# Kernel tuning notes

Hardware: AMD Instinct MI355X
Metric: run time of the kernel (lower is better)

Reference implementation:

```python
import jax, jax.numpy as jnp
import numpy as np

N_NODES = 4096
IN_FEAT = 256
N_HEADS = 8
N_HIDDEN = 32  # out_features // n_heads
NEG_SLOPE = 0.2


def setup_inputs() -> dict:
    key = jax.random.key(0)
    k1, k2, k3, k4 = jax.random.split(key, 4)
    h = jax.random.normal(k1, (N_NODES, IN_FEAT), dtype=jnp.float32)
    W = jax.random.normal(k2, (N_HEADS * N_HIDDEN, IN_FEAT), dtype=jnp.float32) * 0.05
    a = jax.random.normal(k3, (2 * N_HIDDEN,), dtype=jnp.float32) * 0.05
    adj_mat = jax.random.randint(k4, (N_NODES, N_NODES, 1), 0, 2, dtype=jnp.int32)
    return {"h": h, "W": W, "a": a, "adj_mat": adj_mat}


def reference(h, W, a, adj_mat):
    n = h.shape[0]
    # g = linear(h) -> [N, H, F]
    g = (h @ W.T).reshape(n, N_HEADS, N_HIDDEN)
    # e_ij = LeakyReLU(a^T [g_i || g_j]) = LeakyReLU(a_l . g_i + a_r . g_j)
    a_l, a_r = a[:N_HIDDEN], a[N_HIDDEN:]
    s_i = jnp.einsum('nhf,f->nh', g, a_l)  # destination term (repeat_interleave axis)
    s_j = jnp.einsum('nhf,f->nh', g, a_r)  # source term (repeat axis)
    e = jax.nn.leaky_relu(s_i[:, None, :] + s_j[None, :, :], NEG_SLOPE)  # [N, N, H]
    e = jnp.where(adj_mat == 0, jnp.float32(-jnp.inf), e)
    att = jax.nn.softmax(e, axis=1)  # softmax over source nodes j
    # dropout(p) in eval mode -> identity
    out = jnp.einsum('ijh,jhf->ihf', att, g)
    return out.reshape(n, N_HEADS * N_HIDDEN)  # is_concat=True
```

## Files before the change

kernel.cpp:

```cpp
#include <hip/hip_runtime.h>
#include <math.h>

constexpr int N   = 4096;
constexpr int F   = 256;
constexpr int NH  = 8;
constexpr int HID = 32;
constexpr float SLOPE = 0.2f;

using h2       = __attribute__((ext_vector_type(2))) _Float16;
using frag_f16 = __attribute__((ext_vector_type(8))) _Float16;
using frag_cd  = __attribute__((ext_vector_type(4))) float;
using frag_c16 = __attribute__((ext_vector_type(16))) float;

__device__ inline unsigned short f2h(float x) {
  _Float16 v = (_Float16)x;
  unsigned short u; __builtin_memcpy(&u, &v, 2); return u;
}

__global__ __launch_bounds__(256) void k_u(const float* __restrict__ W,
                                           const float* __restrict__ a,
                                           float* __restrict__ U) {
  const int c = blockIdx.x, k = threadIdx.x;
  const int head = c & 7, side = c >> 3;
  float acc = 0.f;
#pragma unroll
  for (int f = 0; f < 32; ++f)
    acc += W[(size_t)(head * 32 + f) * F + k] * a[side * 32 + f];
  U[c * F + k] = acc;
}

__global__ __launch_bounds__(256) void k_front(const float* __restrict__ h,
                                               const float* __restrict__ W,
                                               const float* __restrict__ U,
                                               const int* __restrict__ adj,
                                               unsigned int* __restrict__ RT2,
                                               unsigned short* __restrict__ BT,
                                               unsigned short* __restrict__ DT,
                                               unsigned short* __restrict__ gT,
                                               unsigned int* __restrict__ bits,
                                               float* __restrict__ outp,
                                               float* __restrict__ lbuf) {
  const int b = blockIdx.x, t = threadIdx.x;
  if (b < 256) {
    const int i0 = b * 16;
    const int r = t >> 4, c = t & 15;
    const float4* hp = (const float4*)(h + (size_t)(i0 + r) * F);
    const float4* up = (const float4*)(U + (size_t)c * F);
    float acc = 0.f;
#pragma unroll
    for (int k4 = 0; k4 < 64; ++k4) {
      const float4 hv = hp[k4];
      const float4 uv = up[k4];
      acc += hv.x * uv.x + hv.y * uv.y + hv.z * uv.z + hv.w * uv.w;
    }
    const int n = i0 + r;
    if (c < 8) {
      const unsigned int r16 = f2h(__expf(-0.8f * acc));
      RT2[(size_t)n * NH + c] = (r16 << 16) | r16;
    } else {
      const int hd = c - 8;
      BT[(size_t)hd * N + n] = f2h(__expf(acc));
      DT[(size_t)hd * N + n] = f2h(__expf(SLOPE * acc));
    }
  } else if (b < 1280) {
    const int lane = t & 63;
    const int tile = (b - 256) * 4 + (t >> 6);
    const int mt = tile >> 4, nt = tile & 15;
    const int m0 = mt * 16, n0 = nt * 16;
    const int n16 = lane & 15, quad = lane >> 4;
    frag_cd acc = {0.f, 0.f, 0.f, 0.f};
    const float* ap = h + (size_t)(m0 + n16) * F + quad * 8;
    const float* bp = W + (size_t)(n0 + n16) * F + quad * 8;
#pragma unroll
    for (int ks = 0; ks < F / 32; ++ks) {
      const float4 a0 = *(const float4*)(ap + ks * 32);
      const float4 a1 = *(const float4*)(ap + ks * 32 + 4);
      const float4 b0 = *(const float4*)(bp + ks * 32);
      const float4 b1 = *(const float4*)(bp + ks * 32 + 4);
      const frag_f16 af = {(_Float16)a0.x, (_Float16)a0.y, (_Float16)a0.z, (_Float16)a0.w,
                           (_Float16)a1.x, (_Float16)a1.y, (_Float16)a1.z, (_Float16)a1.w};
      const frag_f16 bf = {(_Float16)b0.x, (_Float16)b0.y, (_Float16)b0.z, (_Float16)b0.w,
                           (_Float16)b1.x, (_Float16)b1.y, (_Float16)b1.z, (_Float16)b1.w};
      acc = __builtin_amdgcn_mfma_f32_16x16x32_f16(af, bf, acc, 0, 0, 0);
    }
    unsigned short tmp[4];
#pragma unroll
    for (int reg = 0; reg < 4; ++reg) tmp[reg] = f2h(acc[reg]);
    *(int2*)(gT + (size_t)(n0 + n16) * N + m0 + quad * 4) = *(int2*)tmp;
  } else if (b < 3328) {
    const int lane = t & 63, w = t >> 6;
    const int row  = (b - 1280) * 2 + (w >> 1);
    const int half = w & 1;
    const int4* arow = (const int4*)(adj + (size_t)row * N) + half * 512;
    unsigned int* brow = bits + (size_t)row * (N / 32) + half * 64;
#pragma unroll
    for (int c = 0; c < 8; ++c) {
      const int4 av = arow[c * 64 + lane];
      unsigned int v = (av.x != 0 ? 1u : 0u) | (av.y != 0 ? 2u : 0u) |
                       (av.z != 0 ? 4u : 0u) | (av.w != 0 ? 8u : 0u);
      v <<= ((lane & 7) * 4);
      v |= __shfl_xor(v, 1);
      v |= __shfl_xor(v, 2);
      v |= __shfl_xor(v, 4);
      if ((lane & 7) == 0) brow[c * 8 + (lane >> 3)] = v;
    }
  } else if (b < 3584) {
    const int base = (b - 3328) * 256 + t;
#pragma unroll
    for (int q = 0; q < 4; ++q)
      *(float4*)(outp + ((size_t)q * 65536 + base) * 4) =
          make_float4(0.f, 0.f, 0.f, 0.f);
  } else {
    *(float4*)(lbuf + ((size_t)(b - 3584) * 256 + t) * 4) =
        make_float4(0.f, 0.f, 0.f, 0.f);
  }
}

constexpr int TI = 64;
constexpr int NSPLIT = 4;

__global__ __launch_bounds__(256, 4) void k_agg(
    const unsigned short* __restrict__ gT,
    const unsigned int* __restrict__ RT2,
    const unsigned short* __restrict__ BT, const unsigned short* __restrict__ DT,
    const unsigned int* __restrict__ bits,
    float* __restrict__ outp, float* __restrict__ lbuf) {
  __shared__ __align__(16) unsigned short sB[64][140];
  __shared__ __align__(16) uint4 sBD[2][2][128];

  const int t    = threadIdx.x;
  const int lane = t & 63;
  const int wv   = t >> 6;
  const int isub = wv & 1;
  const int hd   = wv >> 1;
  const int b    = blockIdx.x;
  const int hp   = b & 3;
  const int js   = (b >> 2) & (NSPLIT - 1);
  const int i0   = (b >> 4) * TI;
  const int head = hp * 2 + hd;

  const int n32 = lane & 31;
  const int kh  = lane >> 5;

  const int myi = i0 + isub * 32 + n32;
  const unsigned int Ri2u = RT2[(size_t)myi * NH + head];
  h2 Ri2; __builtin_memcpy(&Ri2, &Ri2u, 4);
  const uint4* bp4 = (const uint4*)(bits + (size_t)myi * (N / 32) + js * 32);

  frag_c16 acc = {0.f, 0.f, 0.f, 0.f, 0.f, 0.f, 0.f, 0.f,
                  0.f, 0.f, 0.f, 0.f, 0.f, 0.f, 0.f, 0.f};
  float lpart = 0.f;
#if __has_builtin(__builtin_amdgcn_fdot2)
  const h2 one2 = {(_Float16)1.0f, (_Float16)1.0f};
#endif

  const int sr = t >> 2, ss0 = t & 3;
  const unsigned short* gsrc = gT + (size_t)(hp * 64 + sr) * N + js * 1024;

  {
    const int hsel = t >> 7, idx = t & 127;
    sBD[0][hsel][idx] =
        ((const uint4*)(BT + (size_t)(hp * 2 + hsel) * N + js * 1024))[idx];
    sBD[1][hsel][idx] =
        ((const uint4*)(DT + (size_t)(hp * 2 + hsel) * N + js * 1024))[idx];
  }
  {
    int4 pre[4];
#pragma unroll
    for (int s = 0; s < 4; ++s)
      pre[s] = *(const int4*)(gsrc + (ss0 + s * 4) * 8);
#pragma unroll
    for (int s = 0; s < 4; ++s) {
      const int seg = ss0 + s * 4;
      *(int2*)&sB[sr][seg * 8]     = make_int2(pre[s].x, pre[s].y);
      *(int2*)&sB[sr][seg * 8 + 4] = make_int2(pre[s].z, pre[s].w);
    }
  }
  __syncthreads();

  for (int c8 = 0; c8 < 8; ++c8) {
    int4 nxt[4];
    if (c8 < 7) {
#pragma unroll
      for (int s = 0; s < 4; ++s)
        nxt[s] = *(const int4*)(gsrc + (c8 + 1) * 128 + (ss0 + s * 4) * 8);
    }
    const uint4 bw = bp4[c8];
    const unsigned int bwa[4] = {bw.x, bw.y, bw.z, bw.w};
#pragma unroll
    for (int ss = 0; ss < 8; ++ss) {
      const int jb = ss * 16 + kh * 8;
      const uint4 Bv = sBD[0][hd][c8 * 16 + ss * 2 + kh];
      const uint4 Dv = sBD[1][hd][c8 * 16 + ss * 2 + kh];
      const unsigned int mb = (bwa[ss >> 1] >> (((ss & 1) << 4) + (kh << 3))) & 0xFFu;
      const unsigned int bu[4] = {Bv.x, Bv.y, Bv.z, Bv.w};
      const unsigned int du[4] = {Dv.x, Dv.y, Dv.z, Dv.w};
      unsigned int packed[4];
#pragma unroll
      for (int p = 0; p < 4; ++p) {
        h2 hB, hD;
        __builtin_memcpy(&hB, &bu[p], 4);
        __builtin_memcpy(&hD, &du[p], 4);
        const h2 wm = __builtin_elementwise_max(hB, Ri2 * hD);
        unsigned int wp; __builtin_memcpy(&wp, &wm, 4);
        const unsigned int d  = (mb >> (2 * p)) & 3u;
        const unsigned int sp = ((d | (d << 15)) & 0x10001u) * 0xFFFFu;
        wp &= sp;
        packed[p] = wp;
        h2 wh; __builtin_memcpy(&wh, &wp, 4);
#if __has_builtin(__builtin_amdgcn_fdot2)
        lpart = __builtin_amdgcn_fdot2(wh, one2, lpart, false);
#else
        lpart += (float)wh.x + (float)wh.y;
#endif
      }
      frag_f16 af; __builtin_memcpy(&af, packed, 16);

      const int frow = hd * 32 + n32;
      const int2 blo = *(const int2*)&sB[frow][jb];
      const int2 bhi = *(const int2*)&sB[frow][jb + 4];
      const int bt[4] = {blo.x, blo.y, bhi.x, bhi.y};
      frag_f16 bf; __builtin_memcpy(&bf, bt, 16);

      acc = __builtin_amdgcn_mfma_f32_32x32x16_f16(af, bf, acc, 0, 0, 0);
    }
    if (c8 < 7) {
      __syncthreads();
#pragma unroll
      for (int s = 0; s < 4; ++s) {
        const int seg = ss0 + s * 4;
        *(int2*)&sB[sr][seg * 8]     = make_int2(nxt[s].x, nxt[s].y);
        *(int2*)&sB[sr][seg * 8 + 4] = make_int2(nxt[s].z, nxt[s].w);
      }
      __syncthreads();
    }
  }

  const float lp2 = lpart + __shfl_xor(lpart, 32);
  if (kh == 0) atomicAdd(&lbuf[(size_t)myi * NH + head], lp2);
#pragma unroll
  for (int reg = 0; reg < 16; ++reg) {
    const int row = (reg & 3) + 8 * (reg >> 2) + 4 * kh;
    atomicAdd(&outp[(size_t)(i0 + isub * 32 + row) * F + head * HID + n32], acc[reg]);
  }
}

__global__ __launch_bounds__(256) void k_norm(float* __restrict__ outp,
                                              const float* __restrict__ lbuf) {
  const int idx = blockIdx.x * 256 + threadIdx.x;
  const int i = idx >> 6, fq = idx & 63;
  const int hh = fq >> 3;
  const float inv = 1.f / lbuf[(size_t)i * NH + hh];
  float4 v = *(float4*)(outp + (size_t)idx * 4);
  v.x *= inv; v.y *= inv; v.z *= inv; v.w *= inv;
  *(float4*)(outp + (size_t)idx * 4) = v;
}

extern "C" void kernel_launch(void* const* d_in, const int* in_sizes, int n_in,
                              void* d_out, int out_size, void* d_ws, size_t ws_size,
                              hipStream_t stream) {
  const float* h   = (const float*)d_in[0];
  const float* W   = (const float*)d_in[1];
  const float* a   = (const float*)d_in[2];
  const int*   adj = (const int*)d_in[3];
  float* out = (float*)d_out;

  char* ws = (char*)d_ws;
  unsigned short* gT = (unsigned short*)ws;  ws += (size_t)N * F * 2;
  unsigned int* bits = (unsigned int*)ws;    ws += (size_t)N * (N / 32) * 4;
  unsigned int* RT2 = (unsigned int*)ws;     ws += (size_t)N * NH * 4;
  unsigned short* BT = (unsigned short*)ws;  ws += (size_t)N * NH * 2;
  unsigned short* DT = (unsigned short*)ws;  ws += (size_t)N * NH * 2;
  float* lbuf = (float*)ws;                  ws += (size_t)N * NH * 4;
  float* U    = (float*)ws;                  ws += 16 * F * 4;

  k_u<<<dim3(16), dim3(256), 0, stream>>>(W, a, U);
  k_front<<<dim3(3616), dim3(256), 0, stream>>>(h, W, U, adj, RT2, BT, DT, gT,
                                                bits, out, lbuf);
  k_agg<<<dim3((N / TI) * 4 * NSPLIT), dim3(256), 0, stream>>>(
      gT, RT2, BT, DT, bits, out, lbuf);
  k_norm<<<dim3(N * F / 4 / 256), dim3(256), 0, stream>>>(out, lbuf);
}
```

Baseline: 158.8 us.

## Replace atomic accumulation with per-split partial buffers and MFMA row sums

The aggregation kernel now writes per-split partial outputs and softmax denominators to separate buffers with plain stores instead of float atomics. The final normalise kernel sums the four partials before dividing. Denominators are computed by a second MFMA against a ones fragment instead of fdot2 scalar sums. The zero-fill blocks are removed, and adjacency bit-packing is rewritten so each thread loads 32 ints and forms one word without shuffles. This trades atomic contention and zeroing for extra workspace traffic and a doubled MFMA count. The new packing assumes adjacency values are exactly 0 or 1.

```diff
diff --git a/kernel.cpp b/kernel.cpp
--- a/kernel.cpp
+++ b/kernel.cpp
@@ -37,9 +37,7 @@
                                                unsigned short* __restrict__ BT,
                                                unsigned short* __restrict__ DT,
                                                unsigned short* __restrict__ gT,
-                                               unsigned int* __restrict__ bits,
-                                               float* __restrict__ outp,
-                                               float* __restrict__ lbuf) {
+                                               unsigned int* __restrict__ bits) {
   const int b = blockIdx.x, t = threadIdx.x;
   if (b < 256) {
     const int i0 = b * 16;
@@ -87,32 +85,19 @@
 #pragma unroll
     for (int reg = 0; reg < 4; ++reg) tmp[reg] = f2h(acc[reg]);
     *(int2*)(gT + (size_t)(n0 + n16) * N + m0 + quad * 4) = *(int2*)tmp;
-  } else if (b < 3328) {
-    const int lane = t & 63, w = t >> 6;
-    const int row  = (b - 1280) * 2 + (w >> 1);
-    const int half = w & 1;
-    const int4* arow = (const int4*)(adj + (size_t)row * N) + half * 512;
-    unsigned int* brow = bits + (size_t)row * (N / 32) + half * 64;
-#pragma unroll
-    for (int c = 0; c < 8; ++c) {
-      const int4 av = arow[c * 64 + lane];
-      unsigned int v = (av.x != 0 ? 1u : 0u) | (av.y != 0 ? 2u : 0u) |
-                       (av.z != 0 ? 4u : 0u) | (av.w != 0 ? 8u : 0u);
-      v <<= ((lane & 7) * 4);
-      v |= __shfl_xor(v, 1);
-      v |= __shfl_xor(v, 2);
-      v |= __shfl_xor(v, 4);
-      if ((lane & 7) == 0) brow[c * 8 + (lane >> 3)] = v;
-    }
-  } else if (b < 3584) {
-    const int base = (b - 3328) * 256 + t;
-#pragma unroll
-    for (int q = 0; q < 4; ++q)
-      *(float4*)(outp + ((size_t)q * 65536 + base) * 4) =
-          make_float4(0.f, 0.f, 0.f, 0.f);
   } else {
-    *(float4*)(lbuf + ((size_t)(b - 3584) * 256 + t) * 4) =
-        make_float4(0.f, 0.f, 0.f, 0.f);
+    const int row  = (b - 1280) * 2 + (t >> 7);
+    const int word = t & 127;
+    const int4* src = (const int4*)(adj + (size_t)row * N + word * 32);
+    unsigned int wv = 0;
+#pragma unroll
+    for (int q = 0; q < 8; ++q) {
+      const int4 v4 = src[q];
+      const unsigned int nib = (unsigned)v4.x | ((unsigned)v4.y << 1) |
+                               ((unsigned)v4.z << 2) | ((unsigned)v4.w << 3);
+      wv |= nib << (q * 4);
+    }
+    bits[(size_t)row * (N / 32) + word] = wv;
   }
 }
 
@@ -124,7 +109,7 @@
     const unsigned int* __restrict__ RT2,
     const unsigned short* __restrict__ BT, const unsigned short* __restrict__ DT,
     const unsigned int* __restrict__ bits,
-    float* __restrict__ outp, float* __restrict__ lbuf) {
+    float* __restrict__ parts, float* __restrict__ lparts) {
   __shared__ __align__(16) unsigned short sB[64][140];
   __shared__ __align__(16) uint4 sBD[2][2][128];
 
@@ -149,10 +134,11 @@
 
   frag_c16 acc = {0.f, 0.f, 0.f, 0.f, 0.f, 0.f, 0.f, 0.f,
                   0.f, 0.f, 0.f, 0.f, 0.f, 0.f, 0.f, 0.f};
-  float lpart = 0.f;
-#if __has_builtin(__builtin_amdgcn_fdot2)
-  const h2 one2 = {(_Float16)1.0f, (_Float16)1.0f};
-#endif
+  frag_c16 accl = {0.f, 0.f, 0.f, 0.f, 0.f, 0.f, 0.f, 0.f,
+                   0.f, 0.f, 0.f, 0.f, 0.f, 0.f, 0.f, 0.f};
+  frag_f16 fone;
+#pragma unroll
+  for (int u = 0; u < 8; ++u) fone[u] = (_Float16)1.0f;
 
   const int sr = t >> 2, ss0 = t & 3;
   const unsigned short* gsrc = gT + (size_t)(hp * 64 + sr) * N + js * 1024;
@@ -207,12 +193,6 @@
         const unsigned int sp = ((d | (d << 15)) & 0x10001u) * 0xFFFFu;
         wp &= sp;
         packed[p] = wp;
-        h2 wh; __builtin_memcpy(&wh, &wp, 4);
-#if __has_builtin(__builtin_amdgcn_fdot2)
-        lpart = __builtin_amdgcn_fdot2(wh, one2, lpart, false);
-#else
-        lpart += (float)wh.x + (float)wh.y;
-#endif
       }
       frag_f16 af; __builtin_memcpy(&af, packed, 16);
 
@@ -222,7 +202,8 @@
       const int bt[4] = {blo.x, blo.y, bhi.x, bhi.y};
       frag_f16 bf; __builtin_memcpy(&bf, bt, 16);
 
-      acc = __builtin_amdgcn_mfma_f32_32x32x16_f16(af, bf, acc, 0, 0, 0);
+      acc  = __builtin_amdgcn_mfma_f32_32x32x16_f16(af, bf, acc, 0, 0, 0);
+      accl = __builtin_amdgcn_mfma_f32_32x32x16_f16(af, fone, accl, 0, 0, 0);
     }
     if (c8 < 7) {
       __syncthreads();
@@ -236,24 +217,39 @@
     }
   }
 
-  const float lp2 = lpart + __shfl_xor(lpart, 32);
-  if (kh == 0) atomicAdd(&lbuf[(size_t)myi * NH + head], lp2);
+  float* op = parts + (size_t)js * N * F;
 #pragma unroll
   for (int reg = 0; reg < 16; ++reg) {
     const int row = (reg & 3) + 8 * (reg >> 2) + 4 * kh;
-    atomicAdd(&outp[(size_t)(i0 + isub * 32 + row) * F + head * HID + n32], acc[reg]);
-  }
-}
-
-__global__ __launch_bounds__(256) void k_norm(float* __restrict__ outp,
-                                              const float* __restrict__ lbuf) {
+    op[(size_t)(i0 + isub * 32 + row) * F + head * HID + n32] = acc[reg];
+  }
+  if (n32 == 0) {
+    float* lp = lparts + (size_t)js * N * NH;
+#pragma unroll
+    for (int reg = 0; reg < 16; ++reg) {
+      const int row = (reg & 3) + 8 * (reg >> 2) + 4 * kh;
+      lp[(size_t)(i0 + isub * 32 + row) * NH + head] = accl[reg];
+    }
+  }
+}
+
+__global__ __launch_bounds__(256) void k_norm(const float* __restrict__ parts,
+                                              const float* __restrict__ lparts,
+                                              float* __restrict__ out) {
   const int idx = blockIdx.x * 256 + threadIdx.x;
   const int i = idx >> 6, fq = idx & 63;
   const int hh = fq >> 3;
-  const float inv = 1.f / lbuf[(size_t)i * NH + hh];
-  float4 v = *(float4*)(outp + (size_t)idx * 4);
+  float l = 0.f;
+  float4 v = make_float4(0.f, 0.f, 0.f, 0.f);
+#pragma unroll
+  for (int js = 0; js < NSPLIT; ++js) {
+    l += lparts[(size_t)js * N * NH + (size_t)i * NH + hh];
+    const float4 p = *(const float4*)(parts + (size_t)js * N * F + (size_t)idx * 4);
+    v.x += p.x; v.y += p.y; v.z += p.z; v.w += p.w;
+  }
+  const float inv = 1.f / l;
   v.x *= inv; v.y *= inv; v.z *= inv; v.w *= inv;
-  *(float4*)(outp + (size_t)idx * 4) = v;
+  *(float4*)(out + (size_t)idx * 4) = v;
 }
 
 extern "C" void kernel_launch(void* const* d_in, const int* in_sizes, int n_in,
@@ -271,13 +267,13 @@
   unsigned int* RT2 = (unsigned int*)ws;     ws += (size_t)N * NH * 4;
   unsigned short* BT = (unsigned short*)ws;  ws += (size_t)N * NH * 2;
   unsigned short* DT = (unsigned short*)ws;  ws += (size_t)N * NH * 2;
-  float* lbuf = (float*)ws;                  ws += (size_t)N * NH * 4;
   float* U    = (float*)ws;                  ws += 16 * F * 4;
+  float* parts  = (float*)ws;                ws += (size_t)NSPLIT * N * F * 4;
+  float* lparts = (float*)ws;                ws += (size_t)NSPLIT * N * NH * 4;
 
   k_u<<<dim3(16), dim3(256), 0, stream>>>(W, a, U);
-  k_front<<<dim3(3616), dim3(256), 0, stream>>>(h, W, U, adj, RT2, BT, DT, gT,
-                                                bits, out, lbuf);
+  k_front<<<dim3(3328), dim3(256), 0, stream>>>(h, W, U, adj, RT2, BT, DT, gT, bits);
   k_agg<<<dim3((N / TI) * 4 * NSPLIT), dim3(256), 0, stream>>>(
-      gT, RT2, BT, DT, bits, out, lbuf);
-  k_norm<<<dim3(N * F / 4 / 256), dim3(256), 0, stream>>>(out, lbuf);
-}
+      gT, RT2, BT, DT, bits, parts, lparts);
+  k_norm<<<dim3(N * F / 4 / 256), dim3(256), 0, stream>>>(parts, lparts, out);
+}
```

New measurement: 156.5 us. Within noise of the previous version (-1.5%).
